# Performance work log

Hardware: AMD Instinct MI355X
Metric: run time of the kernel (lower is better)

## Reference

```python
import jax, jax.numpy as jnp
import numpy as np

B, D, T = 16, 512, 4096
N_CB, K, CDIM = 9, 1024, 8
EPS = 1e-12  # F.normalize eps


def setup_inputs() -> dict:
    key = jax.random.key(0)
    ks = jax.random.split(key, 6)
    z = jax.random.normal(ks[0], (B, D, T), dtype=jnp.float32)
    # Effective (post weight-norm) 1x1-conv weights per codebook, stacked over N_CB
    w_in = jax.random.normal(ks[1], (N_CB, CDIM, D), dtype=jnp.float32) * 0.02
    b_in = jax.random.normal(ks[2], (N_CB, CDIM), dtype=jnp.float32) * 0.02
    w_out = jax.random.normal(ks[3], (N_CB, D, CDIM), dtype=jnp.float32) * 0.02
    b_out = jax.random.normal(ks[4], (N_CB, D), dtype=jnp.float32) * 0.02
    codebooks = jax.random.normal(ks[5], (N_CB, K, CDIM), dtype=jnp.float32)
    return {"z": z, "w_in": w_in, "b_in": b_in, "w_out": w_out,
            "b_out": b_out, "codebooks": codebooks}


def _l2norm(x):
    return x / jnp.maximum(jnp.linalg.norm(x, axis=-1, keepdims=True), EPS)


def reference(z, w_in, b_in, w_out, b_out, codebooks):
    """Eval-mode RVQ forward with all n_codebooks quantizers (mask all-True).
    Returns (z_q, codes, latents, commitment_loss, codebook_loss)."""
    Bz, _, Tz = z.shape

    def step(carry, params):
        residual, zq_acc, cl, cbl = carry
        wi, bi, wo, bo, cb = params
        # in_proj: 1x1 conv input_dim -> codebook_dim
        z_e = jnp.einsum('cd,bdt->bct', wi, residual) + bi[None, :, None]  # B,CDIM,T
        enc = z_e.transpose(0, 2, 1).reshape(-1, z_e.shape[1])            # (B*T),CDIM
        en = _l2norm(enc)
        cbn = _l2norm(cb)
        # squared euclidean distance on l2-normalized vectors (cosine dist)
        dist = ((en * en).sum(1, keepdims=True)
                - 2.0 * (en @ cbn.T)
                + (cbn * cbn).sum(1)[None, :])                            # (B*T),K
        idx = jnp.argmin(dist, axis=1).reshape(Bz, Tz)                    # B,T
        z_q_i = cb[idx].transpose(0, 2, 1)                                # B,CDIM,T (raw codebook)
        cl = cl + jnp.mean((z_e - jax.lax.stop_gradient(z_q_i)) ** 2, axis=(1, 2)).mean()
        cbl = cbl + jnp.mean((z_q_i - jax.lax.stop_gradient(z_e)) ** 2, axis=(1, 2)).mean()
        # straight-through estimator
        z_q_st = z_e + jax.lax.stop_gradient(z_q_i - z_e)
        z_q_out = jnp.einsum('dc,bct->bdt', wo, z_q_st) + bo[None, :, None]  # B,D,T
        return (residual - z_q_out, zq_acc + z_q_out, cl, cbl), (idx, z_e)

    init = (z, jnp.zeros_like(z), jnp.float32(0.0), jnp.float32(0.0))
    (_, z_q, cl, cbl), (codes, latents) = jax.lax.scan(
        step, init, (w_in, b_in, w_out, b_out, codebooks))
    codes = codes.transpose(1, 0, 2)                         # B,N,T
    latents = latents.transpose(1, 0, 2, 3).reshape(Bz, -1, Tz)  # B,N*CDIM,T
    return z_q, codes, latents, cl, cbl
```

## Files before the change

kernel.cpp:

```cpp
#include <hip/hip_runtime.h>
#include <math.h>

#define Bz  16
#define Dz  512
#define Tz  4096
#define NCB 9
#define Kz  1024
#define CD  8

static const unsigned long long OZQ   = 0ull;
static const unsigned long long OCODE = 33554432ull;
static const unsigned long long OLAT  = 34144256ull;
static const unsigned long long OCL   = 38862848ull;

#define WS_CBN2_OFF (NCB * CD * Kz)

__global__ __launch_bounds__(1024) void rvq_prep(const float* __restrict__ cb,
                                                 float* __restrict__ ws,
                                                 float* __restrict__ out) {
    const int i = blockIdx.x;
    const int k = threadIdx.x;
    const float* row = cb + ((size_t)i * Kz + k) * CD;
    float v[CD];
#pragma unroll
    for (int c = 0; c < CD; ++c) v[c] = row[c];
    float ss = 0.f;
#pragma unroll
    for (int c = 0; c < CD; ++c) ss += v[c] * v[c];
    const float den = fmaxf(sqrtf(ss), 1e-12f);
    float cb2 = 0.f;
#pragma unroll
    for (int c = 0; c < CD; ++c) {
        float e = v[c] / den;
        ws[((size_t)i * CD + c) * Kz + k] = e;
        cb2 += e * e;
    }
    ws[WS_CBN2_OFF + (size_t)i * Kz + k] = cb2;
    if (i == 0 && k == 0) { out[OCL] = 0.f; out[OCL + 1] = 0.f; }
}

template <int CTRL>
__device__ __forceinline__ float dpp_add_t(float v) {
    int t = __builtin_amdgcn_update_dpp(0, __float_as_int(v), CTRL, 0xf, 0xf, true);
    return v + __int_as_float(t);
}
__device__ __forceinline__ float wave_sum64(float v) {
    v = dpp_add_t<0x111>(v);
    v = dpp_add_t<0x112>(v);
    v = dpp_add_t<0x114>(v);
    v = dpp_add_t<0x118>(v);
    v = dpp_add_t<0x142>(v);
    v = dpp_add_t<0x143>(v);
    return __int_as_float(__builtin_amdgcn_readlane(__float_as_int(v), 63));
}
template <int CTRL>
__device__ __forceinline__ float dpp_min_t(float v) {
    int t = __builtin_amdgcn_update_dpp(__float_as_int(v), __float_as_int(v),
                                        CTRL, 0xf, 0xf, false);
    return fminf(v, __int_as_float(t));
}
__device__ __forceinline__ float wave_min64(float v) {
    v = dpp_min_t<0x111>(v);
    v = dpp_min_t<0x112>(v);
    v = dpp_min_t<0x114>(v);
    v = dpp_min_t<0x118>(v);
    v = dpp_min_t<0x142>(v);
    v = dpp_min_t<0x143>(v);
    return __int_as_float(__builtin_amdgcn_readlane(__float_as_int(v), 63));
}
__device__ __forceinline__ float rfl(float v) {
    return __int_as_float(__builtin_amdgcn_readfirstlane(__float_as_int(v)));
}

__global__ __launch_bounds__(1024)
void rvq_main(
    const float* __restrict__ z,
    const float* __restrict__ w_in,
    const float* __restrict__ b_in,
    const float* __restrict__ w_out,
    const float* __restrict__ b_out,
    const float* __restrict__ cb,
    const float* __restrict__ ws,
    float* __restrict__ out)
{
    __shared__ float s_w[CD * 512];
    __shared__ float s_woT[CD * 512];
    __shared__ float s_cbnT[CD * Kz];
    __shared__ float s_cbn2[Kz];
    __shared__ float s_bo[512];
    __shared__ float s_lat[8 * 33];
    __shared__ float s_code[NCB * 32];
    __shared__ float s_red[16];
    float* s_tr = s_cbnT;

    const int tid  = threadIdx.x;
    const int wave = tid >> 6;
    const int lane = tid & 63;
    const int bb   = blockIdx.x;
    const int b    = bb >> 7;
    const int t0blk = (bb & 127) << 5;

    const size_t zbase = (size_t)b * Dz * Tz + t0blk;

    float res2[2][8];
#pragma unroll 1
    for (int c = 0; c < 4; ++c) {
        {
            const int r = tid >> 3;
            const int u = (tid & 7) * 4;
            float4 v = *(const float4*)(z + zbase + (size_t)(c * 128 + r) * Tz + u);
            s_tr[(u + 0) * 132 + r] = v.x;
            s_tr[(u + 1) * 132 + r] = v.y;
            s_tr[(u + 2) * 132 + r] = v.z;
            s_tr[(u + 3) * 132 + r] = v.w;
        }
        __syncthreads();
        if ((lane >> 4) == c) {
            const int lr = (lane & 15) * 8;
#pragma unroll
            for (int col = 0; col < 2; ++col)
#pragma unroll
                for (int j = 0; j < 8; ++j)
                    res2[col][j] = s_tr[(wave * 2 + col) * 132 + lr + j];
        }
        __syncthreads();
    }

    float lsum = 0.f;

#pragma unroll 1
    for (int i = 0; i < NCB; ++i) {
        __syncthreads();
        if (i > 0 && tid < 256) {
            const int c2 = tid >> 5, u = tid & 31;
            out[OLAT + ((size_t)b * 72 + (i - 1) * 8 + c2) * Tz + t0blk + u] =
                s_lat[c2 * 33 + u];
        }
        {
            ((float4*)s_w)[tid] = ((const float4*)(w_in + (size_t)i * 4096))[tid];
            float4 v = ((const float4*)(w_out + (size_t)i * 4096))[tid];
            const int d = tid >> 1, c0 = (tid & 1) * 4;
            s_woT[(c0 + 0) * 512 + d] = v.x;
            s_woT[(c0 + 1) * 512 + d] = v.y;
            s_woT[(c0 + 2) * 512 + d] = v.z;
            s_woT[(c0 + 3) * 512 + d] = v.w;
            const float4* srcT = (const float4*)(ws + (size_t)i * 8192);
            ((float4*)s_cbnT)[tid]        = srcT[tid];
            ((float4*)s_cbnT)[tid + 1024] = srcT[tid + 1024];
            if (tid < 256)
                ((float4*)s_cbn2)[tid] =
                    ((const float4*)(ws + WS_CBN2_OFF + (size_t)i * Kz))[tid];
            if (tid < 128)
                ((float4*)s_bo)[tid] = ((const float4*)(b_out + (size_t)i * Dz))[tid];
        }
        __syncthreads();

        float zz[2][8];
#pragma unroll
        for (int c = 0; c < 8; ++c) {
            float4 wa = *(const float4*)&s_w[c * 512 + lane * 8];
            float4 wc = *(const float4*)&s_w[c * 512 + lane * 8 + 4];
            float q0 = wa.x * res2[0][0];
            float q1 = wa.x * res2[1][0];
            q0 = fmaf(wa.y, res2[0][1], q0); q1 = fmaf(wa.y, res2[1][1], q1);
            q0 = fmaf(wa.z, res2[0][2], q0); q1 = fmaf(wa.z, res2[1][2], q1);
            q0 = fmaf(wa.w, res2[0][3], q0); q1 = fmaf(wa.w, res2[1][3], q1);
            q0 = fmaf(wc.x, res2[0][4], q0); q1 = fmaf(wc.x, res2[1][4], q1);
            q0 = fmaf(wc.y, res2[0][5], q0); q1 = fmaf(wc.y, res2[1][5], q1);
            q0 = fmaf(wc.z, res2[0][6], q0); q1 = fmaf(wc.z, res2[1][6], q1);
            q0 = fmaf(wc.w, res2[0][7], q0); q1 = fmaf(wc.w, res2[1][7], q1);
            zz[0][c] = wave_sum64(q0);
            zz[1][c] = wave_sum64(q1);
        }
        {
            float4 bA = *(const float4*)(b_in + i * 8);
            float4 bB = *(const float4*)(b_in + i * 8 + 4);
            zz[0][0] += bA.x; zz[1][0] += bA.x;
            zz[0][1] += bA.y; zz[1][1] += bA.y;
            zz[0][2] += bA.z; zz[1][2] += bA.z;
            zz[0][3] += bA.w; zz[1][3] += bA.w;
            zz[0][4] += bB.x; zz[1][4] += bB.x;
            zz[0][5] += bB.y; zz[1][5] += bB.y;
            zz[0][6] += bB.z; zz[1][6] += bB.z;
            zz[0][7] += bB.w; zz[1][7] += bB.w;
        }

        {
            float v = zz[0][0];
            v = (lane == 1)  ? zz[1][0] : v;
            v = (lane == 2)  ? zz[0][1] : v;
            v = (lane == 3)  ? zz[1][1] : v;
            v = (lane == 4)  ? zz[0][2] : v;
            v = (lane == 5)  ? zz[1][2] : v;
            v = (lane == 6)  ? zz[0][3] : v;
            v = (lane == 7)  ? zz[1][3] : v;
            v = (lane == 8)  ? zz[0][4] : v;
            v = (lane == 9)  ? zz[1][4] : v;
            v = (lane == 10) ? zz[0][5] : v;
            v = (lane == 11) ? zz[1][5] : v;
            v = (lane == 12) ? zz[0][6] : v;
            v = (lane == 13) ? zz[1][6] : v;
            v = (lane == 14) ? zz[0][7] : v;
            v = (lane == 15) ? zz[1][7] : v;
            if (lane < 16)
                s_lat[(lane >> 1) * 33 + wave * 2 + (lane & 1)] = v;
        }

        float ss0 = 0.f, ss1 = 0.f;
#pragma unroll
        for (int c = 0; c < 8; ++c) {
            ss0 = fmaf(zz[0][c], zz[0][c], ss0);
            ss1 = fmaf(zz[1][c], zz[1][c], ss1);
        }
        const float den0 = fmaxf(sqrtf(ss0), 1e-12f);
        const float den1 = fmaxf(sqrtf(ss1), 1e-12f);
        float en[2][8];
#pragma unroll
        for (int c = 0; c < 8; ++c) {
            en[0][c] = zz[0][c] / den0;
            en[1][c] = zz[1][c] / den1;
        }

        float best0 = 1e30f, best1 = 1e30f;
        int   bi0 = 0, bi1 = 0;
#pragma unroll
        for (int mq = 0; mq < 4; ++mq) {
            const int kb = mq * 256 + lane * 4;
            float4 c2 = *(const float4*)&s_cbn2[kb];
            float d00 = 0.f, d01 = 0.f, d02 = 0.f, d03 = 0.f;
            float d10 = 0.f, d11 = 0.f, d12 = 0.f, d13 = 0.f;
#pragma unroll
            for (int c = 0; c < 8; ++c) {
                float4 v = *(const float4*)&s_cbnT[c * 1024 + kb];
                d00 = fmaf(en[0][c], v.x, d00); d10 = fmaf(en[1][c], v.x, d10);
                d01 = fmaf(en[0][c], v.y, d01); d11 = fmaf(en[1][c], v.y, d11);
                d02 = fmaf(en[0][c], v.z, d02); d12 = fmaf(en[1][c], v.z, d12);
                d03 = fmaf(en[0][c], v.w, d03); d13 = fmaf(en[1][c], v.w, d13);
            }
            float dist;
            dist = fmaf(-2.f, d00, c2.x); if (dist < best0) { best0 = dist; bi0 = kb + 0; }
            dist = fmaf(-2.f, d01, c2.y); if (dist < best0) { best0 = dist; bi0 = kb + 1; }
            dist = fmaf(-2.f, d02, c2.z); if (dist < best0) { best0 = dist; bi0 = kb + 2; }
            dist = fmaf(-2.f, d03, c2.w); if (dist < best0) { best0 = dist; bi0 = kb + 3; }
            dist = fmaf(-2.f, d10, c2.x); if (dist < best1) { best1 = dist; bi1 = kb + 0; }
            dist = fmaf(-2.f, d11, c2.y); if (dist < best1) { best1 = dist; bi1 = kb + 1; }
            dist = fmaf(-2.f, d12, c2.z); if (dist < best1) { best1 = dist; bi1 = kb + 2; }
            dist = fmaf(-2.f, d13, c2.w); if (dist < best1) { best1 = dist; bi1 = kb + 3; }
        }
        const float g0 = wave_min64(best0);
        const float g1 = wave_min64(best1);
        const int wl0 = __ffsll((long long)(unsigned long long)__ballot(best0 == g0)) - 1;
        const int wl1 = __ffsll((long long)(unsigned long long)__ballot(best1 == g1)) - 1;
        const int k0 = __builtin_amdgcn_readlane(bi0, wl0);
        const int k1 = __builtin_amdgcn_readlane(bi1, wl1);

        float cq0[8], cq1[8];
        {
            const float* cr0 = cb + ((size_t)i * Kz + k0) * CD;
            float4 qa = *(const float4*)cr0, qb = *(const float4*)(cr0 + 4);
            cq0[0] = rfl(qa.x); cq0[1] = rfl(qa.y); cq0[2] = rfl(qa.z); cq0[3] = rfl(qa.w);
            cq0[4] = rfl(qb.x); cq0[5] = rfl(qb.y); cq0[6] = rfl(qb.z); cq0[7] = rfl(qb.w);
            const float* cr1 = cb + ((size_t)i * Kz + k1) * CD;
            float4 qc = *(const float4*)cr1, qd = *(const float4*)(cr1 + 4);
            cq1[0] = rfl(qc.x); cq1[1] = rfl(qc.y); cq1[2] = rfl(qc.z); cq1[3] = rfl(qc.w);
            cq1[4] = rfl(qd.x); cq1[5] = rfl(qd.y); cq1[6] = rfl(qd.z); cq1[7] = rfl(qd.w);
        }

        if (lane < 2)
            s_code[i * 32 + wave * 2 + lane] = (lane == 0) ? (float)k0 : (float)k1;

        if (lane == 0) {
#pragma unroll
            for (int c = 0; c < 8; ++c) {
                float dd = zz[0][c] - cq0[c];
                lsum = fmaf(dd, dd, lsum);
            }
        }
        if (lane == 1) {
#pragma unroll
            for (int c = 0; c < 8; ++c) {
                float dd = zz[1][c] - cq1[c];
                lsum = fmaf(dd, dd, lsum);
            }
        }

#pragma unroll
        for (int c = 0; c < 8; ++c) {
            float4 wa = *(const float4*)&s_woT[c * 512 + lane * 8];
            float4 wc = *(const float4*)&s_woT[c * 512 + lane * 8 + 4];
            const float a0 = cq0[c], a1 = cq1[c];
            res2[0][0] = fmaf(-a0, wa.x, res2[0][0]); res2[1][0] = fmaf(-a1, wa.x, res2[1][0]);
            res2[0][1] = fmaf(-a0, wa.y, res2[0][1]); res2[1][1] = fmaf(-a1, wa.y, res2[1][1]);
            res2[0][2] = fmaf(-a0, wa.z, res2[0][2]); res2[1][2] = fmaf(-a1, wa.z, res2[1][2]);
            res2[0][3] = fmaf(-a0, wa.w, res2[0][3]); res2[1][3] = fmaf(-a1, wa.w, res2[1][3]);
            res2[0][4] = fmaf(-a0, wc.x, res2[0][4]); res2[1][4] = fmaf(-a1, wc.x, res2[1][4]);
            res2[0][5] = fmaf(-a0, wc.y, res2[0][5]); res2[1][5] = fmaf(-a1, wc.y, res2[1][5]);
            res2[0][6] = fmaf(-a0, wc.z, res2[0][6]); res2[1][6] = fmaf(-a1, wc.z, res2[1][6]);
            res2[0][7] = fmaf(-a0, wc.w, res2[0][7]); res2[1][7] = fmaf(-a1, wc.w, res2[1][7]);
        }
        {
            float4 bA = *(const float4*)&s_bo[lane * 8];
            float4 bB = *(const float4*)&s_bo[lane * 8 + 4];
            res2[0][0] -= bA.x; res2[1][0] -= bA.x;
            res2[0][1] -= bA.y; res2[1][1] -= bA.y;
            res2[0][2] -= bA.z; res2[1][2] -= bA.z;
            res2[0][3] -= bA.w; res2[1][3] -= bA.w;
            res2[0][4] -= bB.x; res2[1][4] -= bB.x;
            res2[0][5] -= bB.y; res2[1][5] -= bB.y;
            res2[0][6] -= bB.z; res2[1][6] -= bB.z;
            res2[0][7] -= bB.w; res2[1][7] -= bB.w;
        }
    }

    __syncthreads();
    if (tid < 256) {
        const int c2 = tid >> 5, u = tid & 31;
        out[OLAT + ((size_t)b * 72 + 8 * 8 + c2) * Tz + t0blk + u] = s_lat[c2 * 33 + u];
    }
    if (tid < NCB * 32) {
        const int i2 = tid >> 5, u = tid & 31;
        out[OCODE + ((size_t)b * NCB + i2) * Tz + t0blk + u] = s_code[i2 * 32 + u];
    }

#pragma unroll 1
    for (int c = 0; c < 4; ++c) {
        if ((lane >> 4) == c) {
            const int lr = (lane & 15) * 8;
#pragma unroll
            for (int col = 0; col < 2; ++col)
#pragma unroll
                for (int j = 0; j < 8; ++j)
                    s_tr[(wave * 2 + col) * 132 + lr + j] = res2[col][j];
        }
        __syncthreads();
        {
            const int r = tid >> 3;
            const int u = (tid & 7) * 4;
            float4 zv = *(const float4*)(z + zbase + (size_t)(c * 128 + r) * Tz + u);
            float4 v;
            v.x = zv.x - s_tr[(u + 0) * 132 + r];
            v.y = zv.y - s_tr[(u + 1) * 132 + r];
            v.z = zv.z - s_tr[(u + 2) * 132 + r];
            v.w = zv.w - s_tr[(u + 3) * 132 + r];
            *(float4*)(out + OZQ + zbase + (size_t)(c * 128 + r) * Tz + u) = v;
        }
        __syncthreads();
    }

    float lt = wave_sum64(lsum);
    if (lane == 0) s_red[wave] = lt;
    __syncthreads();
    if (tid == 0) {
        float t = 0.f;
#pragma unroll
        for (int w2 = 0; w2 < 16; ++w2) t += s_red[w2];
        t *= (1.f / 524288.f);
        atomicAdd(&out[OCL], t);
        atomicAdd(&out[OCL + 1], t);
    }
}

extern "C" void kernel_launch(void* const* d_in, const int* in_sizes, int n_in,
                              void* d_out, int out_size, void* d_ws, size_t ws_size,
                              hipStream_t stream) {
    (void)in_sizes; (void)n_in; (void)out_size; (void)ws_size;
    const float* z     = (const float*)d_in[0];
    const float* w_in  = (const float*)d_in[1];
    const float* b_in  = (const float*)d_in[2];
    const float* w_out = (const float*)d_in[3];
    const float* b_out = (const float*)d_in[4];
    const float* cb    = (const float*)d_in[5];
    float* ws  = (float*)d_ws;
    float* out = (float*)d_out;

    rvq_prep<<<NCB, 1024, 0, stream>>>(cb, ws, out);
    rvq_main<<<2048, 1024, 0, stream>>>(z, w_in, b_in, w_out, b_out, cb, ws, out);
}
```

Before: 1.348 ms.

## Halve block size to 512 threads, swizzle weight LDS layout, trim zz liveness

Measured after the change: 1.186 ms. 12.0% less time.

```diff
diff --git a/kernel.cpp b/kernel.cpp
--- a/kernel.cpp
+++ b/kernel.cpp
@@ -72,7 +72,7 @@
     return __int_as_float(__builtin_amdgcn_readfirstlane(__float_as_int(v)));
 }
 
-__global__ __launch_bounds__(1024)
+__global__ __launch_bounds__(512)
 void rvq_main(
     const float* __restrict__ z,
     const float* __restrict__ w_in,
@@ -88,26 +88,27 @@
     __shared__ float s_cbnT[CD * Kz];
     __shared__ float s_cbn2[Kz];
     __shared__ float s_bo[512];
-    __shared__ float s_lat[8 * 33];
-    __shared__ float s_code[NCB * 32];
-    __shared__ float s_red[16];
+    __shared__ float s_lat[8 * 17];
+    __shared__ float s_code[NCB * 16];
+    __shared__ float s_red[8];
     float* s_tr = s_cbnT;
 
     const int tid  = threadIdx.x;
     const int wave = tid >> 6;
     const int lane = tid & 63;
     const int bb   = blockIdx.x;
-    const int b    = bb >> 7;
-    const int t0blk = (bb & 127) << 5;
+    const int b    = bb >> 8;
+    const int t0blk = (bb & 255) << 4;
 
     const size_t zbase = (size_t)b * Dz * Tz + t0blk;
+    const int sw = (lane >> 2) & 1;
 
     float res2[2][8];
 #pragma unroll 1
     for (int c = 0; c < 4; ++c) {
         {
-            const int r = tid >> 3;
-            const int u = (tid & 7) * 4;
+            const int r = tid >> 2;
+            const int u = (tid & 3) * 4;
             float4 v = *(const float4*)(z + zbase + (size_t)(c * 128 + r) * Tz + u);
             s_tr[(u + 0) * 132 + r] = v.x;
             s_tr[(u + 1) * 132 + r] = v.y;
@@ -131,48 +132,63 @@
 #pragma unroll 1
     for (int i = 0; i < NCB; ++i) {
         __syncthreads();
-        if (i > 0 && tid < 256) {
-            const int c2 = tid >> 5, u = tid & 31;
+        if (i > 0 && tid < 128) {
+            const int c2 = tid >> 4, u = tid & 15;
             out[OLAT + ((size_t)b * 72 + (i - 1) * 8 + c2) * Tz + t0blk + u] =
-                s_lat[c2 * 33 + u];
-        }
-        {
-            ((float4*)s_w)[tid] = ((const float4*)(w_in + (size_t)i * 4096))[tid];
-            float4 v = ((const float4*)(w_out + (size_t)i * 4096))[tid];
-            const int d = tid >> 1, c0 = (tid & 1) * 4;
-            s_woT[(c0 + 0) * 512 + d] = v.x;
-            s_woT[(c0 + 1) * 512 + d] = v.y;
-            s_woT[(c0 + 2) * 512 + d] = v.z;
-            s_woT[(c0 + 3) * 512 + d] = v.w;
+                s_lat[c2 * 17 + u];
+        }
+        {
             const float4* srcT = (const float4*)(ws + (size_t)i * 8192);
-            ((float4*)s_cbnT)[tid]        = srcT[tid];
-            ((float4*)s_cbnT)[tid + 1024] = srcT[tid + 1024];
+#pragma unroll
+            for (int it = 0; it < 4; ++it)
+                ((float4*)s_cbnT)[tid + it * 512] = srcT[tid + it * 512];
             if (tid < 256)
                 ((float4*)s_cbn2)[tid] =
                     ((const float4*)(ws + WS_CBN2_OFF + (size_t)i * Kz))[tid];
+            const float4* srcW = (const float4*)(w_in + (size_t)i * 4096);
+#pragma unroll
+            for (int it = 0; it < 2; ++it) {
+                const int s = tid + it * 512;
+                ((float4*)s_w)[s ^ ((s >> 3) & 1)] = srcW[s];
+            }
+            const float4* srcO = (const float4*)(w_out + (size_t)i * 4096);
+#pragma unroll
+            for (int it = 0; it < 2; ++it) {
+                const int e4 = tid + it * 512;
+                float4 v = srcO[e4];
+                const int d = e4 >> 1, c0 = (e4 & 1) * 4;
+                const int dsw = d ^ (((d >> 5) & 1) << 2);
+                s_woT[(c0 + 0) * 512 + dsw] = v.x;
+                s_woT[(c0 + 1) * 512 + dsw] = v.y;
+                s_woT[(c0 + 2) * 512 + dsw] = v.z;
+                s_woT[(c0 + 3) * 512 + dsw] = v.w;
+            }
             if (tid < 128)
                 ((float4*)s_bo)[tid] = ((const float4*)(b_out + (size_t)i * Dz))[tid];
         }
         __syncthreads();
 
-        float zz[2][8];
-#pragma unroll
-        for (int c = 0; c < 8; ++c) {
-            float4 wa = *(const float4*)&s_w[c * 512 + lane * 8];
-            float4 wc = *(const float4*)&s_w[c * 512 + lane * 8 + 4];
-            float q0 = wa.x * res2[0][0];
-            float q1 = wa.x * res2[1][0];
-            q0 = fmaf(wa.y, res2[0][1], q0); q1 = fmaf(wa.y, res2[1][1], q1);
-            q0 = fmaf(wa.z, res2[0][2], q0); q1 = fmaf(wa.z, res2[1][2], q1);
-            q0 = fmaf(wa.w, res2[0][3], q0); q1 = fmaf(wa.w, res2[1][3], q1);
-            q0 = fmaf(wc.x, res2[0][4], q0); q1 = fmaf(wc.x, res2[1][4], q1);
-            q0 = fmaf(wc.y, res2[0][5], q0); q1 = fmaf(wc.y, res2[1][5], q1);
-            q0 = fmaf(wc.z, res2[0][6], q0); q1 = fmaf(wc.z, res2[1][6], q1);
-            q0 = fmaf(wc.w, res2[0][7], q0); q1 = fmaf(wc.w, res2[1][7], q1);
-            zz[0][c] = wave_sum64(q0);
-            zz[1][c] = wave_sum64(q1);
-        }
-        {
+        float den0, den1;
+        float en[2][8];
+        {
+            float zz[2][8];
+#pragma unroll
+            for (int c = 0; c < 8; ++c) {
+                const int s0 = c * 128 + lane * 2;
+                float4 wa = ((const float4*)s_w)[s0 + sw];
+                float4 wc = ((const float4*)s_w)[s0 + 1 - sw];
+                float q0 = wa.x * res2[0][0];
+                float q1 = wa.x * res2[1][0];
+                q0 = fmaf(wa.y, res2[0][1], q0); q1 = fmaf(wa.y, res2[1][1], q1);
+                q0 = fmaf(wa.z, res2[0][2], q0); q1 = fmaf(wa.z, res2[1][2], q1);
+                q0 = fmaf(wa.w, res2[0][3], q0); q1 = fmaf(wa.w, res2[1][3], q1);
+                q0 = fmaf(wc.x, res2[0][4], q0); q1 = fmaf(wc.x, res2[1][4], q1);
+                q0 = fmaf(wc.y, res2[0][5], q0); q1 = fmaf(wc.y, res2[1][5], q1);
+                q0 = fmaf(wc.z, res2[0][6], q0); q1 = fmaf(wc.z, res2[1][6], q1);
+                q0 = fmaf(wc.w, res2[0][7], q0); q1 = fmaf(wc.w, res2[1][7], q1);
+                zz[0][c] = wave_sum64(q0);
+                zz[1][c] = wave_sum64(q1);
+            }
             float4 bA = *(const float4*)(b_in + i * 8);
             float4 bB = *(const float4*)(b_in + i * 8 + 4);
             zz[0][0] += bA.x; zz[1][0] += bA.x;
@@ -183,9 +199,7 @@
             zz[0][5] += bB.y; zz[1][5] += bB.y;
             zz[0][6] += bB.z; zz[1][6] += bB.z;
             zz[0][7] += bB.w; zz[1][7] += bB.w;
-        }
-
-        {
+
             float v = zz[0][0];
             v = (lane == 1)  ? zz[1][0] : v;
             v = (lane == 2)  ? zz[0][1] : v;
@@ -203,22 +217,21 @@
             v = (lane == 14) ? zz[0][7] : v;
             v = (lane == 15) ? zz[1][7] : v;
             if (lane < 16)
-                s_lat[(lane >> 1) * 33 + wave * 2 + (lane & 1)] = v;
-        }
-
-        float ss0 = 0.f, ss1 = 0.f;
-#pragma unroll
-        for (int c = 0; c < 8; ++c) {
-            ss0 = fmaf(zz[0][c], zz[0][c], ss0);
-            ss1 = fmaf(zz[1][c], zz[1][c], ss1);
-        }
-        const float den0 = fmaxf(sqrtf(ss0), 1e-12f);
-        const float den1 = fmaxf(sqrtf(ss1), 1e-12f);
-        float en[2][8];
-#pragma unroll
-        for (int c = 0; c < 8; ++c) {
-            en[0][c] = zz[0][c] / den0;
-            en[1][c] = zz[1][c] / den1;
+                s_lat[(lane >> 1) * 17 + wave * 2 + (lane & 1)] = v;
+
+            float ss0 = 0.f, ss1 = 0.f;
+#pragma unroll
+            for (int c = 0; c < 8; ++c) {
+                ss0 = fmaf(zz[0][c], zz[0][c], ss0);
+                ss1 = fmaf(zz[1][c], zz[1][c], ss1);
+            }
+            den0 = fmaxf(sqrtf(ss0), 1e-12f);
+            den1 = fmaxf(sqrtf(ss1), 1e-12f);
+#pragma unroll
+            for (int c = 0; c < 8; ++c) {
+                en[0][c] = zz[0][c] / den0;
+                en[1][c] = zz[1][c] / den1;
+            }
         }
 
         float best0 = 1e30f, best1 = 1e30f;
@@ -267,27 +280,28 @@
         }
 
         if (lane < 2)
-            s_code[i * 32 + wave * 2 + lane] = (lane == 0) ? (float)k0 : (float)k1;
+            s_code[i * 16 + wave * 2 + lane] = (lane == 0) ? (float)k0 : (float)k1;
 
         if (lane == 0) {
 #pragma unroll
             for (int c = 0; c < 8; ++c) {
-                float dd = zz[0][c] - cq0[c];
+                float dd = en[0][c] * den0 - cq0[c];
                 lsum = fmaf(dd, dd, lsum);
             }
         }
         if (lane == 1) {
 #pragma unroll
             for (int c = 0; c < 8; ++c) {
-                float dd = zz[1][c] - cq1[c];
+                float dd = en[1][c] * den1 - cq1[c];
                 lsum = fmaf(dd, dd, lsum);
             }
         }
 
 #pragma unroll
         for (int c = 0; c < 8; ++c) {
-            float4 wa = *(const float4*)&s_woT[c * 512 + lane * 8];
-            float4 wc = *(const float4*)&s_woT[c * 512 + lane * 8 + 4];
+            const int s0 = c * 128 + lane * 2;
+            float4 wa = ((const float4*)s_woT)[s0 + sw];
+            float4 wc = ((const float4*)s_woT)[s0 + 1 - sw];
             const float a0 = cq0[c], a1 = cq1[c];
             res2[0][0] = fmaf(-a0, wa.x, res2[0][0]); res2[1][0] = fmaf(-a1, wa.x, res2[1][0]);
             res2[0][1] = fmaf(-a0, wa.y, res2[0][1]); res2[1][1] = fmaf(-a1, wa.y, res2[1][1]);
@@ -313,13 +327,13 @@
     }
 
     __syncthreads();
-    if (tid < 256) {
-        const int c2 = tid >> 5, u = tid & 31;
-        out[OLAT + ((size_t)b * 72 + 8 * 8 + c2) * Tz + t0blk + u] = s_lat[c2 * 33 + u];
-    }
-    if (tid < NCB * 32) {
-        const int i2 = tid >> 5, u = tid & 31;
-        out[OCODE + ((size_t)b * NCB + i2) * Tz + t0blk + u] = s_code[i2 * 32 + u];
+    if (tid < 128) {
+        const int c2 = tid >> 4, u = tid & 15;
+        out[OLAT + ((size_t)b * 72 + 8 * 8 + c2) * Tz + t0blk + u] = s_lat[c2 * 17 + u];
+    }
+    if (tid < NCB * 16) {
+        const int i2 = tid >> 4, u = tid & 15;
+        out[OCODE + ((size_t)b * NCB + i2) * Tz + t0blk + u] = s_code[i2 * 16 + u];
     }
 
 #pragma unroll 1
@@ -334,8 +348,8 @@
         }
         __syncthreads();
         {
-            const int r = tid >> 3;
-            const int u = (tid & 7) * 4;
+            const int r = tid >> 2;
+            const int u = (tid & 3) * 4;
             float4 zv = *(const float4*)(z + zbase + (size_t)(c * 128 + r) * Tz + u);
             float4 v;
             v.x = zv.x - s_tr[(u + 0) * 132 + r];
@@ -353,7 +367,7 @@
     if (tid == 0) {
         float t = 0.f;
 #pragma unroll
-        for (int w2 = 0; w2 < 16; ++w2) t += s_red[w2];
+        for (int w2 = 0; w2 < 8; ++w2) t += s_red[w2];
         t *= (1.f / 524288.f);
         atomicAdd(&out[OCL], t);
         atomicAdd(&out[OCL + 1], t);
@@ -374,5 +388,5 @@
     float* out = (float*)d_out;
 
     rvq_prep<<<NCB, 1024, 0, stream>>>(cb, ws, out);
-    rvq_main<<<2048, 1024, 0, stream>>>(z, w_in, b_in, w_out, b_out, cb, ws, out);
-}
+    rvq_main<<<4096, 512, 0, stream>>>(z, w_in, b_in, w_out, b_out, cb, ws, out);
+}
```
